# Optimization experiments

Hardware: AMD Instinct MI355X
Metric: run time of the kernel (lower is better)

## Reference

```python
import jax, jax.numpy as jnp
import numpy as np

B, NV, RN, SN = 1, 4, 1024, 128
H = W = 256
C_FEAT = 32   # img_feat_dim
D_VIEW = 32   # view transformer d_model
PE_D = 8      # PE_d_hid
D_RAY = D_VIEW + PE_D  # 40
NHEAD = 8
EPS_LN = 1e-5


def _layernorm(x, g, b):
    m = x.mean(-1, keepdims=True)
    v = ((x - m) ** 2).mean(-1, keepdims=True)
    return (x - m) * jax.lax.rsqrt(v + EPS_LN) * g + b


def _linear_attention(q, k, v):
    # LoFTR kernelized linear attention; q,k,v: (n, L, h, d)
    Q = jax.nn.elu(q) + 1.0
    K = jax.nn.elu(k) + 1.0
    L = v.shape[1]
    KV = jnp.einsum('nshd,nshv->nhdv', K, v / L)
    Z = 1.0 / (jnp.einsum('nlhd,nhd->nlh', Q, K.sum(axis=1)) + 1e-6)
    return jnp.einsum('nlhd,nhdv,nlh->nlhv', Q, KV, Z) * L


def _loftr_self_layer(x, Wq, Wk, Wv, Wm, g1, b1, W1, W2, g2, b2):
    # LoFTREncoderLayer with self-attention (x is both query and source)
    n, L, d = x.shape
    dim = d // NHEAD
    q = (x @ Wq).reshape(n, L, NHEAD, dim)
    k = (x @ Wk).reshape(n, L, NHEAD, dim)
    v = (x @ Wv).reshape(n, L, NHEAD, dim)
    msg = _linear_attention(q, k, v).reshape(n, L, d) @ Wm
    msg = _layernorm(msg, g1, b1)
    msg = jax.nn.relu(jnp.concatenate([x, msg], -1) @ W1) @ W2
    msg = _layernorm(msg, g2, b2)
    return x + msg


def _grid_sample_2d(img, pix):
    # img: (N,C,H,W); pix: (N,RN,SN,2) in pixel coords.
    # bilinear, align_corners=True, zero padding; mask = in-bounds.
    N, C, Hh, Ww = img.shape
    x, y = pix[..., 0], pix[..., 1]
    mask = ((x >= 0) & (x <= Ww - 1) & (y >= 0) & (y <= Hh - 1)).astype(img.dtype)
    x0 = jnp.floor(x)
    y0 = jnp.floor(y)
    flat = img.reshape(N, C, Hh * Ww)

    def gather(ix, iy):
        valid = ((ix >= 0) & (ix < Ww) & (iy >= 0) & (iy < Hh)).astype(img.dtype)
        idx = (jnp.clip(iy, 0, Hh - 1) * Ww + jnp.clip(ix, 0, Ww - 1)).astype(jnp.int32)
        out = jnp.take_along_axis(flat, idx.reshape(N, 1, -1), axis=2)
        return out.reshape(N, C, ix.shape[1], ix.shape[2]) * valid[:, None]

    wx1 = x - x0
    wy1 = y - y0
    out = (gather(x0, y0) * ((1 - wx1) * (1 - wy1))[:, None]
           + gather(x0 + 1, y0) * (wx1 * (1 - wy1))[:, None]
           + gather(x0, y0 + 1) * ((1 - wx1) * wy1)[:, None]
           + gather(x0 + 1, y0 + 1) * (wx1 * wy1)[:, None])
    return out, mask


def _order_posenc(d_hid, n):
    pos = np.arange(n)[:, None].astype(np.float64)
    j = np.arange(d_hid)[None, :]
    tab = pos / np.power(10000.0, 2 * (j // 2) / d_hid)
    tab[:, 0::2] = np.sin(tab[:, 0::2])
    tab[:, 1::2] = np.cos(tab[:, 1::2])
    return jnp.asarray(tab, dtype=jnp.float32)


def _forward(point3D, source_imgs, source_imgs_feat, ref_pose_inv, source_poses_inv,
             source_poses, view_token,
             vt_Wq, vt_Wk, vt_Wv, vt_Wm, vt_g1, vt_b1, vt_W1, vt_W2, vt_g2, vt_b2,
             rt_Wq, rt_Wk, rt_Wv, rt_Wm, rt_g1, rt_b1, rt_W1, rt_W2, rt_g2, rt_b2,
             dm_W1, dm_b1, dm_W2, dm_b2, dm_W3, dm_b3,
             rw_W1, rw_b1, rw_W2, rw_b2, rw_W3, rw_b3):
    b, nv, _, h, w = source_imgs.shape
    _, rn, sn, _ = point3D.shape

    # relative viewing directions (B,NV,RN,SN,3)
    v1 = point3D - ref_pose_inv[:, None, None, :3, -1]
    v2 = point3D[:, None] - source_poses_inv[:, :, None, None, :3, -1]
    v1 = v1 / jnp.linalg.norm(v1, axis=-1, keepdims=True)
    v2 = v2 / jnp.linalg.norm(v2, axis=-1, keepdims=True)
    dir_relative = v1[:, None] - v2

    # project points into all source views: (B,NV,3,RN,SN)
    pts_h = jnp.concatenate([point3D, jnp.ones_like(point3D[..., :1])], -1)
    pip = jnp.einsum('bnij,brsj->bnirs', source_poses, pts_h)[:, :, :3]
    mask_valid_depth = (pip[:, :, 2] > 0).astype(point3D.dtype)
    pix = pip[:, :, :2] / pip[:, :, 2:3]
    grid = jnp.moveaxis(pix, 2, -1).reshape(b * nv, rn, sn, 2)

    feat_s, mask = _grid_sample_2d(source_imgs_feat.reshape(b * nv, -1, h, w), grid)
    rgb_s, _ = _grid_sample_2d(source_imgs.reshape(b * nv, -1, h, w), grid)
    mask = mask.reshape(b, nv, rn, sn) * mask_valid_depth

    # per-point multi-view tokens: (B*RN*SN, NV, C)
    x = feat_s.reshape(b, nv, -1, rn, sn).transpose(0, 3, 4, 1, 2).reshape(b * rn * sn, nv, -1)
    tok = jnp.broadcast_to(view_token, (x.shape[0], 1, view_token.shape[-1]))
    x = jnp.concatenate([tok, x], axis=1)  # prepend view token -> L = NV+1
    x = _loftr_self_layer(x, vt_Wq, vt_Wk, vt_Wv, vt_Wm, vt_g1, vt_b1, vt_W1, vt_W2, vt_g2, vt_b2)

    x1 = jnp.moveaxis(x, 1, 0)          # (NV+1, B*RN*SN, C)
    view_feature = x1[1:]
    x = x1[0].reshape(b * rn, sn, -1)   # token output per sample along ray

    pe = _order_posenc(PE_D, sn)        # (SN, 8)
    x = jnp.concatenate([x, jnp.broadcast_to(pe, (b * rn, sn, PE_D))], -1)
    x = _loftr_self_layer(x, rt_Wq, rt_Wk, rt_Wv, rt_Wm, rt_g1, rt_b1, rt_W1, rt_W2, rt_g2, rt_b2)

    hdm = jax.nn.relu(x @ dm_W1 + dm_b1)
    hdm = jax.nn.relu(hdm @ dm_W2 + dm_b2)
    srdf = hdm @ dm_W3 + dm_b3           # (B*RN, SN, 1)

    # radiance blending weights over views
    vf = view_feature.reshape(nv, b, rn, sn, -1).transpose(1, 2, 3, 0, 4)  # (B,RN,SN,NV,C)
    dr = dir_relative.transpose(0, 2, 3, 1, 4)                             # (B,RN,SN,NV,3)
    xw = jnp.concatenate([vf, dr], -1)
    xw = jax.nn.relu(xw @ rw_W1 + rw_b1)
    xw = jax.nn.relu(xw @ rw_W2 + rw_b2)
    xw = xw @ rw_W3 + rw_b3                                                # (B,RN,SN,NV,1)
    m = mask.transpose(0, 2, 3, 1)[..., None]
    xw = jnp.where(m == 0, -1e9, xw)
    weight = jax.nn.softmax(xw, axis=-2)
    w_bn = weight[..., 0].transpose(0, 3, 1, 2)[:, :, None]                # (B,NV,1,RN,SN)
    radiance = (rgb_s.reshape(b, nv, 3, rn, sn) * w_bn).sum(axis=1)        # (B,3,RN,SN)
    radiance = radiance.transpose(0, 2, 3, 1).reshape(b * rn * sn, 3)
    return radiance, srdf, pip


def setup_inputs() -> dict:
    key = jax.random.key(0)
    ks = jax.random.split(key, 4)
    u = jax.random.uniform(ks[0], (B, RN, SN, 3), dtype=jnp.float32)
    point3D = jnp.concatenate([u[..., :2] - 0.5, u[..., 2:] + 1.0], -1)  # x,y in [-.5,.5], z in [1,2]
    source_imgs = jax.random.normal(ks[1], (B, NV, 3, H, W), dtype=jnp.float32) * 0.5
    source_imgs_feat = jax.random.normal(ks[2], (B, NV, C_FEAT, H, W), dtype=jnp.float32) * 0.5

    f = 200.0
    P = np.array([[f, 0, W / 2, 0], [0, f, H / 2, 0], [0, 0, 1, 0], [0, 0, 0, 1]], np.float32)
    source_poses = jnp.asarray(np.broadcast_to(P, (B, NV, 4, 4)).copy())
    ref_pose_inv = jnp.asarray(np.broadcast_to(np.eye(4, dtype=np.float32), (B, 4, 4)).copy())
    spi = np.broadcast_to(np.eye(4, dtype=np.float32), (B, NV, 4, 4)).copy()
    spi[:, :, 0, 3] = np.linspace(-0.2, 0.2, NV, dtype=np.float32)  # camera centers
    source_poses_inv = jnp.asarray(spi)

    pk = jax.random.split(ks[3], 20)

    def lin(k, i, o):
        return jax.random.normal(k, (i, o), dtype=jnp.float32) * 0.05

    d, dr = D_VIEW, D_RAY
    params = dict(
        view_token=jax.random.normal(pk[0], (1, d), dtype=jnp.float32),
        vt_Wq=lin(pk[1], d, d), vt_Wk=lin(pk[2], d, d), vt_Wv=lin(pk[3], d, d), vt_Wm=lin(pk[4], d, d),
        vt_g1=jnp.ones(d), vt_b1=jnp.zeros(d),
        vt_W1=lin(pk[5], 2 * d, 2 * d), vt_W2=lin(pk[6], 2 * d, d),
        vt_g2=jnp.ones(d), vt_b2=jnp.zeros(d),
        rt_Wq=lin(pk[7], dr, dr), rt_Wk=lin(pk[8], dr, dr), rt_Wv=lin(pk[9], dr, dr), rt_Wm=lin(pk[10], dr, dr),
        rt_g1=jnp.ones(dr), rt_b1=jnp.zeros(dr),
        rt_W1=lin(pk[11], 2 * dr, 2 * dr), rt_W2=lin(pk[12], 2 * dr, dr),
        rt_g2=jnp.ones(dr), rt_b2=jnp.zeros(dr),
        dm_W1=lin(pk[13], dr, 32), dm_b1=jnp.zeros(32),
        dm_W2=lin(pk[14], 32, 16), dm_b2=jnp.zeros(16),
        dm_W3=lin(pk[15], 16, 1), dm_b3=jnp.zeros(1),
        rw_W1=lin(pk[16], d + 3, 16), rw_b1=jnp.zeros(16),
        rw_W2=lin(pk[17], 16, 8), rw_b2=jnp.zeros(8),
        rw_W3=lin(pk[18], 8, 1), rw_b3=jnp.zeros(1),
    )
    out = dict(point3D=point3D, source_imgs=source_imgs, source_imgs_feat=source_imgs_feat,
               ref_pose_inv=ref_pose_inv, source_poses_inv=source_poses_inv,
               source_poses=source_poses)
    out.update(params)
    return out


def reference(point3D, source_imgs, source_imgs_feat, ref_pose_inv, source_poses_inv,
              source_poses, view_token,
              vt_Wq, vt_Wk, vt_Wv, vt_Wm, vt_g1, vt_b1, vt_W1, vt_W2, vt_g2, vt_b2,
              rt_Wq, rt_Wk, rt_Wv, rt_Wm, rt_g1, rt_b1, rt_W1, rt_W2, rt_g2, rt_b2,
              dm_W1, dm_b1, dm_W2, dm_b2, dm_W3, dm_b3,
              rw_W1, rw_b1, rw_W2, rw_b2, rw_W3, rw_b3):
    return _forward(point3D, source_imgs, source_imgs_feat, ref_pose_inv, source_poses_inv,
                    source_poses, view_token,
                    vt_Wq, vt_Wk, vt_Wv, vt_Wm, vt_g1, vt_b1, vt_W1, vt_W2, vt_g2, vt_b2,
                    rt_Wq, rt_Wk, rt_Wv, rt_Wm, rt_g1, rt_b1, rt_W1, rt_W2, rt_g2, rt_b2,
                    dm_W1, dm_b1, dm_W2, dm_b2, dm_W3, dm_b3,
                    rw_W1, rw_b1, rw_W2, rw_b2, rw_W3, rw_b3)
```

## Files before the change

kernel.cpp:

```cpp
#include <hip/hip_runtime.h>
#include <math.h>

#define NPTS   131072
#define NVIEW  4
#define IMH    256
#define IMW    256

#define WS_FEATT   0u
#define WS_IMGT    8388608u
#define WS_X1      9437184u
#define WS_XR      26214400u
#define WS_MSG     31457280u
#define WS_RGB     36700160u
#define WS_DIR     38273024u
#define WS_MASK    39845888u

__device__ __forceinline__ float elup1(float t) { return t > 0.f ? t + 1.f : expf(t); }

__global__ __launch_bounds__(256) void k0_transpose(
    const float* __restrict__ feat, const float* __restrict__ img,
    float* __restrict__ featT, float* __restrict__ imgT)
{
    int tid = blockIdx.x * 256 + threadIdx.x;
    int v = tid >> 16, pix = tid & 65535;
    float buf[32];
#pragma unroll
    for (int c = 0; c < 32; ++c)
        buf[c] = feat[((size_t)(v * 32 + c) << 16) + pix];
    float4* dst = (float4*)(featT + ((size_t)tid << 5));
#pragma unroll
    for (int q = 0; q < 8; ++q)
        dst[q] = make_float4(buf[4*q], buf[4*q+1], buf[4*q+2], buf[4*q+3]);
    float4 rgb;
    rgb.x = img[((size_t)(v * 3 + 0) << 16) + pix];
    rgb.y = img[((size_t)(v * 3 + 1) << 16) + pix];
    rgb.z = img[((size_t)(v * 3 + 2) << 16) + pix];
    rgb.w = 0.f;
    *(float4*)(imgT + ((size_t)tid << 2)) = rgb;
}

__global__ __launch_bounds__(256) void k1_geom_sample(
    const float* __restrict__ p3d, const float* __restrict__ rpi,
    const float* __restrict__ spi, const float* __restrict__ sp,
    const float* __restrict__ featT, const float* __restrict__ imgT,
    float* __restrict__ x1, float* __restrict__ rgbw,
    float* __restrict__ dirw, float* __restrict__ maskw,
    float* __restrict__ outpip)
{
    int tid = blockIdx.x * 256 + threadIdx.x;
    int p = tid >> 2, v = tid & 3;
    float X = p3d[p * 3 + 0], Y = p3d[p * 3 + 1], Z = p3d[p * 3 + 2];

    float a0 = X - rpi[3], a1 = Y - rpi[7], a2 = Z - rpi[11];
    float na = sqrtf(a0 * a0 + a1 * a1 + a2 * a2);
    a0 /= na; a1 /= na; a2 /= na;
    const float* sv = spi + v * 16;
    float b0 = X - sv[3], b1 = Y - sv[7], b2 = Z - sv[11];
    float nb = sqrtf(b0 * b0 + b1 * b1 + b2 * b2);
    b0 /= nb; b1 /= nb; b2 /= nb;
    dirw[(size_t)p * 12 + v * 3 + 0] = a0 - b0;
    dirw[(size_t)p * 12 + v * 3 + 1] = a1 - b1;
    dirw[(size_t)p * 12 + v * 3 + 2] = a2 - b2;

    const float* P = sp + v * 16;
    float pip0 = P[0] * X + P[1] * Y + P[2]  * Z + P[3];
    float pip1 = P[4] * X + P[5] * Y + P[6]  * Z + P[7];
    float pip2 = P[8] * X + P[9] * Y + P[10] * Z + P[11];
    outpip[(size_t)(v * 3 + 0) * NPTS + p] = pip0;
    outpip[(size_t)(v * 3 + 1) * NPTS + p] = pip1;
    outpip[(size_t)(v * 3 + 2) * NPTS + p] = pip2;

    float gx = pip0 / pip2, gy = pip1 / pip2;
    float inb = (gx >= 0.f && gx <= 255.f && gy >= 0.f && gy <= 255.f) ? 1.f : 0.f;
    float mvd = pip2 > 0.f ? 1.f : 0.f;
    maskw[(size_t)p * 4 + v] = inb * mvd;

    float x0f = floorf(gx), y0f = floorf(gy);
    float wx = gx - x0f, wy = gy - y0f;
    int ix0 = (int)x0f, iy0 = (int)y0f;
    float tw[4] = { (1.f-wx)*(1.f-wy), wx*(1.f-wy), (1.f-wx)*wy, wx*wy };
    int tdx[4] = { 0, 1, 0, 1 };
    int tdy[4] = { 0, 0, 1, 1 };

    float facc[32];
#pragma unroll
    for (int c = 0; c < 32; ++c) facc[c] = 0.f;
    float r0 = 0.f, r1 = 0.f, r2 = 0.f;

#pragma unroll
    for (int tno = 0; tno < 4; ++tno) {
        int ix = ix0 + tdx[tno], iy = iy0 + tdy[tno];
        float valid = (ix >= 0 && ix < IMW && iy >= 0 && iy < IMH) ? 1.f : 0.f;
        int cx = min(max(ix, 0), IMW - 1), cy = min(max(iy, 0), IMH - 1);
        float wgt = tw[tno] * valid;
        size_t base = ((size_t)v << 16) + ((size_t)cy << 8) + (size_t)cx;
        const float4* fp = (const float4*)(featT + base * 32);
#pragma unroll
        for (int q = 0; q < 8; ++q) {
            float4 f4 = fp[q];
            facc[4*q+0] += f4.x * wgt; facc[4*q+1] += f4.y * wgt;
            facc[4*q+2] += f4.z * wgt; facc[4*q+3] += f4.w * wgt;
        }
        float4 rp = *(const float4*)(imgT + base * 4);
        r0 += rp.x * wgt; r1 += rp.y * wgt; r2 += rp.z * wgt;
    }

    float4* xd = (float4*)(x1 + ((size_t)p * 4 + v) * 32);
#pragma unroll
    for (int q = 0; q < 8; ++q)
        xd[q] = make_float4(facc[4*q], facc[4*q+1], facc[4*q+2], facc[4*q+3]);
    rgbw[(size_t)p * 12 + v * 3 + 0] = r0;
    rgbw[(size_t)p * 12 + v * 3 + 1] = r1;
    rgbw[(size_t)p * 12 + v * 3 + 2] = r2;
}

#define K2_BLK    128
#define K2_PTS    24
#define K2_GRID   1024
#define K2_NGRP   ((NPTS + K2_PTS - 1) / K2_PTS)

__device__ __forceinline__ void fma4(const float4 xv, const float* __restrict__ w,
                                     const int stride, float* __restrict__ acc)
{
#pragma unroll
    for (int j = 0; j < 32; ++j) acc[j] = fmaf(xv.x, w[j],            acc[j]);
#pragma unroll
    for (int j = 0; j < 32; ++j) acc[j] = fmaf(xv.y, w[stride + j],   acc[j]);
#pragma unroll
    for (int j = 0; j < 32; ++j) acc[j] = fmaf(xv.z, w[2*stride + j], acc[j]);
#pragma unroll
    for (int j = 0; j < 32; ++j) acc[j] = fmaf(xv.w, w[3*stride + j], acc[j]);
}

__global__ __launch_bounds__(K2_BLK) void k2_loftr1(
    float* __restrict__ x1g, const float* __restrict__ vtok,
    const float* __restrict__ Wq, const float* __restrict__ Wk,
    const float* __restrict__ Wv, const float* __restrict__ Wm,
    const float* __restrict__ g1v, const float* __restrict__ b1v,
    const float* __restrict__ W1, const float* __restrict__ W2,
    const float* __restrict__ g2v, const float* __restrict__ b2v,
    float* __restrict__ xr)
{
    __shared__ float shr[8192];

    int t = threadIdx.x;
    int pl = t / 5, l = t - pl * 5;
    bool act = (t < K2_PTS * 5);
    if (!act) { pl = 0; l = 0; }
    const int rowbase = (pl * 5 + l) * 68;

    for (int grp = blockIdx.x; grp < K2_NGRP; grp += gridDim.x) {
        int p = grp * K2_PTS + pl;
        bool valid = act && (p < NPTS);
        int pload = p < NPTS ? p : NPTS - 1;
        const float4* xsrc = (l == 0) ? (const float4*)vtok
                                      : (const float4*)(x1g + ((size_t)pload * 4 + (l - 1)) * 32);

        __syncthreads();

        {
            float acc[32];
#pragma unroll
            for (int j = 0; j < 32; ++j) acc[j] = 0.f;
            for (int g = 0; g < 8; ++g) {
                float4 xv = xsrc[g];
                fma4(xv, &Wk[g * 128], 32, acc);
            }
            if (act) {
                float* krow = &shr[rowbase];
#pragma unroll
                for (int j = 0; j < 32; j += 4)
                    *(float4*)&krow[j] = make_float4(elup1(acc[j]), elup1(acc[j+1]),
                                                     elup1(acc[j+2]), elup1(acc[j+3]));
            }
        }
        {
            float acc[32];
#pragma unroll
            for (int j = 0; j < 32; ++j) acc[j] = 0.f;
            for (int g = 0; g < 8; ++g) {
                float4 xv = xsrc[g];
                fma4(xv, &Wv[g * 128], 32, acc);
            }
            if (act) {
                float* vrow = &shr[rowbase + 32];
#pragma unroll
                for (int j = 0; j < 32; j += 4)
                    *(float4*)&vrow[j] = make_float4(acc[j], acc[j+1], acc[j+2], acc[j+3]);
            }
        }
        __syncthreads();

        float macc[32];
#pragma unroll
        for (int j = 0; j < 32; ++j) macc[j] = 0.f;
        for (int h = 0; h < 8; ++h) {
            float q0 = 0.f, q1 = 0.f, q2 = 0.f, q3 = 0.f;
            for (int g = 0; g < 8; ++g) {
                float4 xv = xsrc[g];
                const float* w = &Wq[g * 128 + h * 4];
                q0 = fmaf(xv.x, w[0],  q0); q1 = fmaf(xv.x, w[1],  q1);
                q2 = fmaf(xv.x, w[2],  q2); q3 = fmaf(xv.x, w[3],  q3);
                q0 = fmaf(xv.y, w[32], q0); q1 = fmaf(xv.y, w[33], q1);
                q2 = fmaf(xv.y, w[34], q2); q3 = fmaf(xv.y, w[35], q3);
                q0 = fmaf(xv.z, w[64], q0); q1 = fmaf(xv.z, w[65], q1);
                q2 = fmaf(xv.z, w[66], q2); q3 = fmaf(xv.z, w[67], q3);
                q0 = fmaf(xv.w, w[96], q0); q1 = fmaf(xv.w, w[97], q1);
                q2 = fmaf(xv.w, w[98], q2); q3 = fmaf(xv.w, w[99], q3);
            }
            q0 = elup1(q0); q1 = elup1(q1); q2 = elup1(q2); q3 = elup1(q3);

            float kvm[16] = {0,0,0,0,0,0,0,0,0,0,0,0,0,0,0,0};
            float ks0 = 0.f, ks1 = 0.f, ks2 = 0.f, ks3 = 0.f;
#pragma unroll
            for (int l2 = 0; l2 < 5; ++l2) {
                const float* row = &shr[(pl * 5 + l2) * 68 + h * 4];
                float4 K4 = *(const float4*)row;
                float4 V4 = *(const float4*)(row + 32);
                kvm[0]  = fmaf(K4.x, V4.x, kvm[0]);  kvm[1]  = fmaf(K4.x, V4.y, kvm[1]);
                kvm[2]  = fmaf(K4.x, V4.z, kvm[2]);  kvm[3]  = fmaf(K4.x, V4.w, kvm[3]);
                kvm[4]  = fmaf(K4.y, V4.x, kvm[4]);  kvm[5]  = fmaf(K4.y, V4.y, kvm[5]);
                kvm[6]  = fmaf(K4.y, V4.z, kvm[6]);  kvm[7]  = fmaf(K4.y, V4.w, kvm[7]);
                kvm[8]  = fmaf(K4.z, V4.x, kvm[8]);  kvm[9]  = fmaf(K4.z, V4.y, kvm[9]);
                kvm[10] = fmaf(K4.z, V4.z, kvm[10]); kvm[11] = fmaf(K4.z, V4.w, kvm[11]);
                kvm[12] = fmaf(K4.w, V4.x, kvm[12]); kvm[13] = fmaf(K4.w, V4.y, kvm[13]);
                kvm[14] = fmaf(K4.w, V4.z, kvm[14]); kvm[15] = fmaf(K4.w, V4.w, kvm[15]);
                ks0 += K4.x; ks1 += K4.y; ks2 += K4.z; ks3 += K4.w;
            }
            float den = 1e-6f + q0*ks0 + q1*ks1 + q2*ks2 + q3*ks3;
            float inv = 1.f / den;
            float o0 = (q0*kvm[0] + q1*kvm[4] + q2*kvm[8]  + q3*kvm[12]) * inv;
            float o1 = (q0*kvm[1] + q1*kvm[5] + q2*kvm[9]  + q3*kvm[13]) * inv;
            float o2 = (q0*kvm[2] + q1*kvm[6] + q2*kvm[10] + q3*kvm[14]) * inv;
            float o3 = (q0*kvm[3] + q1*kvm[7] + q2*kvm[11] + q3*kvm[15]) * inv;

            const float* wm = &Wm[h * 4 * 32];
#pragma unroll
            for (int j = 0; j < 32; ++j) macc[j] = fmaf(o0, wm[j],      macc[j]);
#pragma unroll
            for (int j = 0; j < 32; ++j) macc[j] = fmaf(o1, wm[32 + j], macc[j]);
#pragma unroll
            for (int j = 0; j < 32; ++j) macc[j] = fmaf(o2, wm[64 + j], macc[j]);
#pragma unroll
            for (int j = 0; j < 32; ++j) macc[j] = fmaf(o3, wm[96 + j], macc[j]);
        }

        float msg[32];
        {
            float s1 = 0.f, s2 = 0.f;
#pragma unroll
            for (int j = 0; j < 32; ++j) { s1 += macc[j]; s2 += macc[j] * macc[j]; }
            float m  = s1 * (1.f / 32.f);
            float va = s2 * (1.f / 32.f) - m * m;
            float rs = rsqrtf(va + 1e-5f);
#pragma unroll
            for (int j = 0; j < 32; ++j)
                msg[j] = (macc[j] - m) * rs * g1v[j] + b1v[j];
        }
        __syncthreads();

#pragma unroll
        for (int g = 0; g < 8; ++g)
            *(float4*)&shr[(g * K2_BLK + t) * 4] =
                make_float4(msg[4*g], msg[4*g+1], msg[4*g+2], msg[4*g+3]);

        float oacc[32];
#pragma unroll
        for (int j = 0; j < 32; ++j) oacc[j] = 0.f;
        for (int half = 0; half < 2; ++half) {
            const int j0 = half * 32;
            float hacc[32];
#pragma unroll
            for (int j = 0; j < 32; ++j) hacc[j] = 0.f;
            for (int g = 0; g < 8; ++g) {
                float4 xv = xsrc[g];
                fma4(xv, &W1[(g * 4) * 64 + j0], 64, hacc);
            }
            for (int g = 0; g < 8; ++g) {
                float4 mv = *(const float4*)&shr[(g * K2_BLK + t) * 4];
                fma4(mv, &W1[(32 + g * 4) * 64 + j0], 64, hacc);
            }
#pragma unroll
            for (int j = 0; j < 32; j += 4)
                *(float4*)&shr[4096 + ((j >> 2) * K2_BLK + t) * 4] =
                    make_float4(fmaxf(hacc[j], 0.f),   fmaxf(hacc[j+1], 0.f),
                                fmaxf(hacc[j+2], 0.f), fmaxf(hacc[j+3], 0.f));
            for (int g = 0; g < 8; ++g) {
                float4 hv = *(const float4*)&shr[4096 + (g * K2_BLK + t) * 4];
                fma4(hv, &W2[(j0 + g * 4) * 32], 32, oacc);
            }
        }

        {
            float s1 = 0.f, s2 = 0.f;
#pragma unroll
            for (int j = 0; j < 32; ++j) { s1 += oacc[j]; s2 += oacc[j] * oacc[j]; }
            float m  = s1 * (1.f / 32.f);
            float va = s2 * (1.f / 32.f) - m * m;
            float rs = rsqrtf(va + 1e-5f);

            if (valid) {
                float y[32];
#pragma unroll
                for (int g = 0; g < 8; ++g) {
                    float4 x4 = xsrc[g];
                    y[4*g] = x4.x; y[4*g+1] = x4.y; y[4*g+2] = x4.z; y[4*g+3] = x4.w;
                }
#pragma unroll
                for (int j = 0; j < 32; ++j)
                    y[j] += (oacc[j] - m) * rs * g2v[j] + b2v[j];

                if (l == 0) {
                    float4* dst = (float4*)(xr + (size_t)p * 40);
#pragma unroll
                    for (int g = 0; g < 8; ++g)
                        dst[g] = make_float4(y[4*g], y[4*g+1], y[4*g+2], y[4*g+3]);
                    int sidx = p & 127;
#pragma unroll
                    for (int c = 0; c < 8; ++c) {
                        float den = (c < 2) ? 1.f : (c < 4) ? 10.f : (c < 6) ? 100.f : 1000.f;
                        float arg = (float)sidx / den;
                        xr[(size_t)p * 40 + 32 + c] = (c & 1) ? cosf(arg) : sinf(arg);
                    }
                } else {
                    float4* dst = (float4*)(x1g + ((size_t)p * 4 + (l - 1)) * 32);
#pragma unroll
                    for (int g = 0; g < 8; ++g)
                        dst[g] = make_float4(y[4*g], y[4*g+1], y[4*g+2], y[4*g+3]);
                }
            }
        }
    }
}

__global__ __launch_bounds__(320) void k3a_attn(
    const float* __restrict__ xr,
    const float* __restrict__ Wq, const float* __restrict__ Wk,
    const float* __restrict__ Wv, const float* __restrict__ Wm,
    const float* __restrict__ g1, const float* __restrict__ b1,
    float* __restrict__ msg)
{
    __shared__ float kb[5120];
    __shared__ float vb[5120];
    __shared__ float wb[1600];
    __shared__ float kvb[200];
    __shared__ float ksb[40];
    int t = threadIdx.x, r = blockIdx.x;
    const float* xbase = xr + (size_t)r * 5120;
    int lg = t / 40, c = t % 40;

    for (int i = t; i < 1600; i += 320) wb[i] = Wk[i];
    __syncthreads();
    {
        float acc[16];
#pragma unroll
        for (int i = 0; i < 16; ++i) acc[i] = 0.f;
        for (int kk = 0; kk < 40; ++kk) {
            float w = wb[kk * 40 + c];
#pragma unroll
            for (int i = 0; i < 16; ++i) acc[i] += xbase[(lg * 16 + i) * 40 + kk] * w;
        }
#pragma unroll
        for (int i = 0; i < 16; ++i) kb[(lg * 16 + i) * 40 + c] = elup1(acc[i]);
    }
    __syncthreads();
    for (int i = t; i < 1600; i += 320) wb[i] = Wv[i];
    __syncthreads();
    {
        float acc[16];
#pragma unroll
        for (int i = 0; i < 16; ++i) acc[i] = 0.f;
        for (int kk = 0; kk < 40; ++kk) {
            float w = wb[kk * 40 + c];
#pragma unroll
            for (int i = 0; i < 16; ++i) acc[i] += xbase[(lg * 16 + i) * 40 + kk] * w;
        }
#pragma unroll
        for (int i = 0; i < 16; ++i) vb[(lg * 16 + i) * 40 + c] = acc[i];
    }
    __syncthreads();
    if (t < 200) {
        int h = t / 25, e = (t / 5) % 5, d = t % 5;
        float kv = 0.f, ks = 0.f;
        for (int s2 = 0; s2 < 128; ++s2) {
            float kvv = kb[s2 * 40 + h * 5 + e];
            float vv  = vb[s2 * 40 + h * 5 + d];
            kv += kvv * vv; ks += kvv;
        }
        kvb[t] = kv;
        if (d == 0) ksb[h * 5 + e] = ks;
    }
    __syncthreads();
    for (int i = t; i < 1600; i += 320) wb[i] = Wq[i];
    __syncthreads();
    {
        float acc[16];
#pragma unroll
        for (int i = 0; i < 16; ++i) acc[i] = 0.f;
        for (int kk = 0; kk < 40; ++kk) {
            float w = wb[kk * 40 + c];
#pragma unroll
            for (int i = 0; i < 16; ++i) acc[i] += xbase[(lg * 16 + i) * 40 + kk] * w;
        }
#pragma unroll
        for (int i = 0; i < 16; ++i) kb[(lg * 16 + i) * 40 + c] = elup1(acc[i]);
    }
    __syncthreads();
    {
        int h = c / 5, d = c % 5;
#pragma unroll 4
        for (int i = 0; i < 16; ++i) {
            int l = lg * 16 + i;
            float den = 1e-6f, o = 0.f;
#pragma unroll
            for (int e = 0; e < 5; ++e) {
                float q = kb[l * 40 + h * 5 + e];
                den += q * ksb[h * 5 + e];
                o   += q * kvb[h * 25 + e * 5 + d];
            }
            vb[l * 40 + c] = o / den;
        }
    }
    __syncthreads();
    for (int i = t; i < 1600; i += 320) wb[i] = Wm[i];
    __syncthreads();
    {
        float acc[16];
#pragma unroll
        for (int i = 0; i < 16; ++i) acc[i] = 0.f;
        for (int kk = 0; kk < 40; ++kk) {
            float w = wb[kk * 40 + c];
#pragma unroll
            for (int i = 0; i < 16; ++i) acc[i] += vb[(lg * 16 + i) * 40 + kk] * w;
        }
#pragma unroll
        for (int i = 0; i < 16; ++i) kb[(lg * 16 + i) * 40 + c] = acc[i];
    }
    __syncthreads();
    if (t < 128) {
        float s1 = 0.f, s2v = 0.f;
        for (int j = 0; j < 40; ++j) { float x = kb[t * 40 + j]; s1 += x; s2v += x * x; }
        float m = s1 * (1.f / 40.f), va = s2v * (1.f / 40.f) - m * m;
        float rs = rsqrtf(va + 1e-5f);
        for (int j = 0; j < 40; ++j)
            msg[((size_t)r * 128 + t) * 40 + j] = (kb[t * 40 + j] - m) * rs * g1[j] + b1[j];
    }
}

__global__ __launch_bounds__(320) void k3b_ffn(
    float* __restrict__ xr, const float* __restrict__ msg,
    const float* __restrict__ W1, const float* __restrict__ W2,
    const float* __restrict__ g2, const float* __restrict__ b2)
{
    __shared__ float hb[10240];
    __shared__ float wb[3200];
    int t = threadIdx.x, r = blockIdx.x;
    int lg = t / 40, c = t % 40;
    const float* xbase = xr + (size_t)r * 5120;
    const float* mbase = msg + (size_t)r * 5120;

    float hA[16], hB[16];
#pragma unroll
    for (int i = 0; i < 16; ++i) { hA[i] = 0.f; hB[i] = 0.f; }

    for (int i = t; i < 3200; i += 320) wb[i] = W1[i];
    __syncthreads();
    for (int kk = 0; kk < 40; ++kk) {
        float wa = wb[kk * 80 + c], wbb = wb[kk * 80 + c + 40];
#pragma unroll
        for (int i = 0; i < 16; ++i) {
            float xv = xbase[(lg * 16 + i) * 40 + kk];
            hA[i] += xv * wa; hB[i] += xv * wbb;
        }
    }
    __syncthreads();
    for (int i = t; i < 3200; i += 320) wb[i] = W1[3200 + i];
    __syncthreads();
    for (int kk = 0; kk < 40; ++kk) {
        float wa = wb[kk * 80 + c], wbb = wb[kk * 80 + c + 40];
#pragma unroll
        for (int i = 0; i < 16; ++i) {
            float mv = mbase[(lg * 16 + i) * 40 + kk];
            hA[i] += mv * wa; hB[i] += mv * wbb;
        }
    }
#pragma unroll
    for (int i = 0; i < 16; ++i) {
        hb[(lg * 16 + i) * 80 + c]      = fmaxf(hA[i], 0.f);
        hb[(lg * 16 + i) * 80 + c + 40] = fmaxf(hB[i], 0.f);
    }
    __syncthreads();
    for (int i = t; i < 3200; i += 320) wb[i] = W2[i];
    __syncthreads();
    float oa[16];
#pragma unroll
    for (int i = 0; i < 16; ++i) oa[i] = 0.f;
    for (int kk = 0; kk < 80; ++kk) {
        float w = wb[kk * 40 + c];
#pragma unroll
        for (int i = 0; i < 16; ++i) oa[i] += hb[(lg * 16 + i) * 80 + kk] * w;
    }
    __syncthreads();
#pragma unroll
    for (int i = 0; i < 16; ++i) hb[(lg * 16 + i) * 40 + c] = oa[i];
    __syncthreads();
    if (t < 128) {
        float s1 = 0.f, s2v = 0.f;
        for (int j = 0; j < 40; ++j) { float x = hb[t * 40 + j]; s1 += x; s2v += x * x; }
        float m = s1 * (1.f / 40.f), va = s2v * (1.f / 40.f) - m * m;
        float rs = rsqrtf(va + 1e-5f);
        for (int j = 0; j < 40; ++j) {
            float y = xbase[t * 40 + j] + (hb[t * 40 + j] - m) * rs * g2[j] + b2[j];
            xr[(size_t)r * 5120 + t * 40 + j] = y;
        }
    }
}

__global__ __launch_bounds__(256) void k4_dm(
    const float* __restrict__ xr,
    const float* __restrict__ W1, const float* __restrict__ b1,
    const float* __restrict__ W2, const float* __restrict__ b2,
    const float* __restrict__ W3, const float* __restrict__ b3,
    float* __restrict__ out1)
{
    __shared__ float s[1857];
    int t = threadIdx.x;
    for (int i = t; i < 1280; i += 256) s[i] = W1[i];
    if (t < 32) s[1280 + t] = b1[t];
    for (int i = t; i < 512; i += 256) s[1312 + i] = W2[i];
    if (t < 16) { s[1824 + t] = b2[t]; s[1840 + t] = W3[t]; }
    if (t == 0) s[1856] = b3[0];
    __syncthreads();

    int p = blockIdx.x * 256 + t;
    float x[40];
    const float4* xp = (const float4*)(xr + (size_t)p * 40);
#pragma unroll
    for (int i = 0; i < 10; ++i) {
        float4 v4 = xp[i];
        x[4*i] = v4.x; x[4*i+1] = v4.y; x[4*i+2] = v4.z; x[4*i+3] = v4.w;
    }
    float h1[32];
#pragma unroll
    for (int j = 0; j < 32; ++j) h1[j] = s[1280 + j];
    for (int k = 0; k < 40; ++k) {
        float xv = x[k];
#pragma unroll
        for (int j = 0; j < 32; ++j) h1[j] += xv * s[k * 32 + j];
    }
#pragma unroll
    for (int j = 0; j < 32; ++j) h1[j] = fmaxf(h1[j], 0.f);
    float h2[16];
#pragma unroll
    for (int j = 0; j < 16; ++j) h2[j] = s[1824 + j];
    for (int k = 0; k < 32; ++k) {
        float hv = h1[k];
#pragma unroll
        for (int j = 0; j < 16; ++j) h2[j] += hv * s[1312 + k * 16 + j];
    }
    float o = s[1856];
#pragma unroll
    for (int j = 0; j < 16; ++j) o += fmaxf(h2[j], 0.f) * s[1840 + j];
    out1[p] = o;
}

__global__ __launch_bounds__(256) void k5_rw(
    const float* __restrict__ vf, const float* __restrict__ dirw,
    const float* __restrict__ maskw, const float* __restrict__ rgbw,
    const float* __restrict__ W1, const float* __restrict__ b1,
    const float* __restrict__ W2, const float* __restrict__ b2,
    const float* __restrict__ W3, const float* __restrict__ b3,
    float* __restrict__ out0)
{
    __shared__ float s[721];
    int t = threadIdx.x;
    for (int i = t; i < 560; i += 256) s[i] = W1[i];
    if (t < 16) s[560 + t] = b1[t];
    if (t < 128) s[576 + t] = W2[t];
    if (t < 8) { s[704 + t] = b2[t]; s[712 + t] = W3[t]; }
    if (t == 0) s[720] = b3[0];
    __syncthreads();

    int p = blockIdx.x * 256 + t;
    float xw[4];
#pragma unroll
    for (int v = 0; v < 4; ++v) {
        float in[35];
        const float4* vp = (const float4*)(vf + ((size_t)p * 4 + v) * 32);
#pragma unroll
        for (int q = 0; q < 8; ++q) {
            float4 f4 = vp[q];
            in[4*q] = f4.x; in[4*q+1] = f4.y; in[4*q+2] = f4.z; in[4*q+3] = f4.w;
        }
        in[32] = dirw[(size_t)p * 12 + v * 3 + 0];
        in[33] = dirw[(size_t)p * 12 + v * 3 + 1];
        in[34] = dirw[(size_t)p * 12 + v * 3 + 2];
        float h1[16];
#pragma unroll
        for (int j = 0; j < 16; ++j) h1[j] = s[560 + j];
        for (int k = 0; k < 35; ++k) {
            float xv = in[k];
#pragma unroll
            for (int j = 0; j < 16; ++j) h1[j] += xv * s[k * 16 + j];
        }
        float h2[8];
#pragma unroll
        for (int j = 0; j < 8; ++j) h2[j] = s[704 + j];
        for (int k = 0; k < 16; ++k) {
            float hv = fmaxf(h1[k], 0.f);
#pragma unroll
            for (int j = 0; j < 8; ++j) h2[j] += hv * s[576 + k * 8 + j];
        }
        float o = s[720];
#pragma unroll
        for (int j = 0; j < 8; ++j) o += fmaxf(h2[j], 0.f) * s[712 + j];
        xw[v] = (maskw[(size_t)p * 4 + v] == 0.f) ? -1e9f : o;
    }
    float m = fmaxf(fmaxf(xw[0], xw[1]), fmaxf(xw[2], xw[3]));
    float e0 = expf(xw[0] - m), e1 = expf(xw[1] - m), e2 = expf(xw[2] - m), e3 = expf(xw[3] - m);
    float inv = 1.f / (e0 + e1 + e2 + e3);
    float w4[4] = { e0 * inv, e1 * inv, e2 * inv, e3 * inv };
    float r0 = 0.f, r1 = 0.f, r2 = 0.f;
#pragma unroll
    for (int v = 0; v < 4; ++v) {
        r0 += rgbw[(size_t)p * 12 + v * 3 + 0] * w4[v];
        r1 += rgbw[(size_t)p * 12 + v * 3 + 1] * w4[v];
        r2 += rgbw[(size_t)p * 12 + v * 3 + 2] * w4[v];
    }
    out0[(size_t)p * 3 + 0] = r0;
    out0[(size_t)p * 3 + 1] = r1;
    out0[(size_t)p * 3 + 2] = r2;
}

extern "C" void kernel_launch(void* const* d_in, const int* in_sizes, int n_in,
                              void* d_out, int out_size, void* d_ws, size_t ws_size,
                              hipStream_t stream) {
    (void)in_sizes; (void)n_in; (void)out_size; (void)ws_size;
    const float* p3d   = (const float*)d_in[0];
    const float* imgs  = (const float*)d_in[1];
    const float* feat  = (const float*)d_in[2];
    const float* rpi   = (const float*)d_in[3];
    const float* spi   = (const float*)d_in[4];
    const float* sp    = (const float*)d_in[5];
    const float* vtok  = (const float*)d_in[6];
    const float* vtWq  = (const float*)d_in[7];
    const float* vtWk  = (const float*)d_in[8];
    const float* vtWv  = (const float*)d_in[9];
    const float* vtWm  = (const float*)d_in[10];
    const float* vtg1  = (const float*)d_in[11];
    const float* vtb1  = (const float*)d_in[12];
    const float* vtW1  = (const float*)d_in[13];
    const float* vtW2  = (const float*)d_in[14];
    const float* vtg2  = (const float*)d_in[15];
    const float* vtb2  = (const float*)d_in[16];
    const float* rtWq  = (const float*)d_in[17];
    const float* rtWk  = (const float*)d_in[18];
    const float* rtWv  = (const float*)d_in[19];
    const float* rtWm  = (const float*)d_in[20];
    const float* rtg1  = (const float*)d_in[21];
    const float* rtb1  = (const float*)d_in[22];
    const float* rtW1  = (const float*)d_in[23];
    const float* rtW2  = (const float*)d_in[24];
    const float* rtg2  = (const float*)d_in[25];
    const float* rtb2  = (const float*)d_in[26];
    const float* dmW1  = (const float*)d_in[27];
    const float* dmb1  = (const float*)d_in[28];
    const float* dmW2  = (const float*)d_in[29];
    const float* dmb2  = (const float*)d_in[30];
    const float* dmW3  = (const float*)d_in[31];
    const float* dmb3  = (const float*)d_in[32];
    const float* rwW1  = (const float*)d_in[33];
    const float* rwb1  = (const float*)d_in[34];
    const float* rwW2  = (const float*)d_in[35];
    const float* rwb2  = (const float*)d_in[36];
    const float* rwW3  = (const float*)d_in[37];
    const float* rwb3  = (const float*)d_in[38];

    float* out  = (float*)d_out;
    float* out0 = out;
    float* out1 = out + 393216;
    float* out2 = out + 524288;

    float* ws    = (float*)d_ws;
    float* featT = ws + WS_FEATT;
    float* imgT  = ws + WS_IMGT;
    float* x1    = ws + WS_X1;
    float* xr    = ws + WS_XR;
    float* msg   = ws + WS_MSG;
    float* rgbw  = ws + WS_RGB;
    float* dirw  = ws + WS_DIR;
    float* maskw = ws + WS_MASK;

    k0_transpose<<<dim3(1024), dim3(256), 0, stream>>>(feat, imgs, featT, imgT);
    k1_geom_sample<<<dim3(2048), dim3(256), 0, stream>>>(p3d, rpi, spi, sp, featT, imgT,
                                                         x1, rgbw, dirw, maskw, out2);
    k2_loftr1<<<dim3(K2_GRID), dim3(K2_BLK), 0, stream>>>(x1, vtok, vtWq, vtWk, vtWv, vtWm,
                                                    vtg1, vtb1, vtW1, vtW2, vtg2, vtb2, xr);
    k3a_attn<<<dim3(1024), dim3(320), 0, stream>>>(xr, rtWq, rtWk, rtWv, rtWm, rtg1, rtb1, msg);
    k3b_ffn<<<dim3(1024), dim3(320), 0, stream>>>(xr, msg, rtW1, rtW2, rtg2, rtb2);
    k4_dm<<<dim3(512), dim3(256), 0, stream>>>(xr, dmW1, dmb1, dmW2, dmb2, dmW3, dmb3, out1);
    k5_rw<<<dim3(512), dim3(256), 0, stream>>>(x1, dirw, maskw, rgbw,
                                               rwW1, rwb1, rwW2, rwb2, rwW3, rwb3, out0);
}
```

Measured before the change: 1.130 ms.

## Restructure ray-transformer attention and FFN kernels to one thread per sample

Rewrites k3a_attn and k3b_ffn so each thread owns one sample and holds its 40-wide rows in registers, doing the projections with wave-uniform weight loads from global/scalar memory instead of staging weights in LDS. K and V are written transposed into padded LDS so the per-head KV reduction can use float4 reads. Block size drops from 320 to 128 threads, and most syncthreads and LDS traffic are removed. In exchange, register pressure rises sharply (arrays of 40 floats, with two or three live at once) and weights are re-read per thread, which may cut occupancy.

```diff
diff --git a/kernel.cpp b/kernel.cpp
--- a/kernel.cpp
+++ b/kernel.cpp
@@ -130,6 +130,19 @@
     for (int j = 0; j < 32; ++j) acc[j] = fmaf(xv.z, w[2*stride + j], acc[j]);
 #pragma unroll
     for (int j = 0; j < 32; ++j) acc[j] = fmaf(xv.w, w[3*stride + j], acc[j]);
+}
+
+__device__ __forceinline__ void fma40(const float4 xv, const float* __restrict__ w,
+                                      const int stride, float* __restrict__ acc)
+{
+#pragma unroll
+    for (int j = 0; j < 40; ++j) acc[j] = fmaf(xv.x, w[j],            acc[j]);
+#pragma unroll
+    for (int j = 0; j < 40; ++j) acc[j] = fmaf(xv.y, w[stride + j],   acc[j]);
+#pragma unroll
+    for (int j = 0; j < 40; ++j) acc[j] = fmaf(xv.z, w[2*stride + j], acc[j]);
+#pragma unroll
+    for (int j = 0; j < 40; ++j) acc[j] = fmaf(xv.w, w[3*stride + j], acc[j]);
 }
 
 __global__ __launch_bounds__(K2_BLK) void k2_loftr1(
@@ -333,186 +346,177 @@
     }
 }
 
-__global__ __launch_bounds__(320) void k3a_attn(
+#define KT_STRIDE 132
+__global__ __launch_bounds__(128) void k3a_attn(
     const float* __restrict__ xr,
     const float* __restrict__ Wq, const float* __restrict__ Wk,
     const float* __restrict__ Wv, const float* __restrict__ Wm,
     const float* __restrict__ g1, const float* __restrict__ b1,
     float* __restrict__ msg)
 {
-    __shared__ float kb[5120];
-    __shared__ float vb[5120];
-    __shared__ float wb[1600];
+    __shared__ float KT[40 * KT_STRIDE];
+    __shared__ float VT[40 * KT_STRIDE];
     __shared__ float kvb[200];
     __shared__ float ksb[40];
+
     int t = threadIdx.x, r = blockIdx.x;
-    const float* xbase = xr + (size_t)r * 5120;
-    int lg = t / 40, c = t % 40;
-
-    for (int i = t; i < 1600; i += 320) wb[i] = Wk[i];
+    const float4* x4 = (const float4*)(xr + ((size_t)r * 128 + t) * 40);
+
+    {
+        float acc[40];
+#pragma unroll
+        for (int j = 0; j < 40; ++j) acc[j] = 0.f;
+        for (int g = 0; g < 10; ++g)
+            fma40(x4[g], &Wk[g * 160], 40, acc);
+#pragma unroll
+        for (int j = 0; j < 40; ++j) KT[j * KT_STRIDE + t] = elup1(acc[j]);
+    }
+    {
+        float acc[40];
+#pragma unroll
+        for (int j = 0; j < 40; ++j) acc[j] = 0.f;
+        for (int g = 0; g < 10; ++g)
+            fma40(x4[g], &Wv[g * 160], 40, acc);
+#pragma unroll
+        for (int j = 0; j < 40; ++j) VT[j * KT_STRIDE + t] = acc[j];
+    }
     __syncthreads();
+
     {
-        float acc[16];
-#pragma unroll
-        for (int i = 0; i < 16; ++i) acc[i] = 0.f;
-        for (int kk = 0; kk < 40; ++kk) {
-            float w = wb[kk * 40 + c];
-#pragma unroll
-            for (int i = 0; i < 16; ++i) acc[i] += xbase[(lg * 16 + i) * 40 + kk] * w;
-        }
-#pragma unroll
-        for (int i = 0; i < 16; ++i) kb[(lg * 16 + i) * 40 + c] = elup1(acc[i]);
+        int lane = t & 63, wid = t >> 6;
+        if (lane < 20) {
+            int idx = wid * 20 + lane;
+            int h = idx / 5;
+            float ks = 0.f;
+            float kv0 = 0.f, kv1 = 0.f, kv2 = 0.f, kv3 = 0.f, kv4 = 0.f;
+            const float* kr = &KT[idx * KT_STRIDE];
+            const float* v0 = &VT[(h * 5 + 0) * KT_STRIDE];
+            const float* v1 = &VT[(h * 5 + 1) * KT_STRIDE];
+            const float* v2 = &VT[(h * 5 + 2) * KT_STRIDE];
+            const float* v3 = &VT[(h * 5 + 3) * KT_STRIDE];
+            const float* v4 = &VT[(h * 5 + 4) * KT_STRIDE];
+            for (int s = 0; s < 128; s += 4) {
+                float4 K4 = *(const float4*)&kr[s];
+                float4 A = *(const float4*)&v0[s];
+                float4 B = *(const float4*)&v1[s];
+                float4 C = *(const float4*)&v2[s];
+                float4 D = *(const float4*)&v3[s];
+                float4 E = *(const float4*)&v4[s];
+                ks  += K4.x + K4.y + K4.z + K4.w;
+                kv0 += K4.x*A.x + K4.y*A.y + K4.z*A.z + K4.w*A.w;
+                kv1 += K4.x*B.x + K4.y*B.y + K4.z*B.z + K4.w*B.w;
+                kv2 += K4.x*C.x + K4.y*C.y + K4.z*C.z + K4.w*C.w;
+                kv3 += K4.x*D.x + K4.y*D.y + K4.z*D.z + K4.w*D.w;
+                kv4 += K4.x*E.x + K4.y*E.y + K4.z*E.z + K4.w*E.w;
+            }
+            ksb[idx] = ks;
+            kvb[idx * 5 + 0] = kv0; kvb[idx * 5 + 1] = kv1;
+            kvb[idx * 5 + 2] = kv2; kvb[idx * 5 + 3] = kv3;
+            kvb[idx * 5 + 4] = kv4;
+        }
     }
     __syncthreads();
-    for (int i = t; i < 1600; i += 320) wb[i] = Wv[i];
-    __syncthreads();
+
+    float o[40];
     {
-        float acc[16];
-#pragma unroll
-        for (int i = 0; i < 16; ++i) acc[i] = 0.f;
-        for (int kk = 0; kk < 40; ++kk) {
-            float w = wb[kk * 40 + c];
-#pragma unroll
-            for (int i = 0; i < 16; ++i) acc[i] += xbase[(lg * 16 + i) * 40 + kk] * w;
-        }
-#pragma unroll
-        for (int i = 0; i < 16; ++i) vb[(lg * 16 + i) * 40 + c] = acc[i];
-    }
-    __syncthreads();
-    if (t < 200) {
-        int h = t / 25, e = (t / 5) % 5, d = t % 5;
-        float kv = 0.f, ks = 0.f;
-        for (int s2 = 0; s2 < 128; ++s2) {
-            float kvv = kb[s2 * 40 + h * 5 + e];
-            float vv  = vb[s2 * 40 + h * 5 + d];
-            kv += kvv * vv; ks += kvv;
-        }
-        kvb[t] = kv;
-        if (d == 0) ksb[h * 5 + e] = ks;
-    }
-    __syncthreads();
-    for (int i = t; i < 1600; i += 320) wb[i] = Wq[i];
-    __syncthreads();
+        float q[40];
+#pragma unroll
+        for (int j = 0; j < 40; ++j) q[j] = 0.f;
+        for (int g = 0; g < 10; ++g)
+            fma40(x4[g], &Wq[g * 160], 40, q);
+#pragma unroll
+        for (int j = 0; j < 40; ++j) q[j] = elup1(q[j]);
+
+#pragma unroll
+        for (int h = 0; h < 8; ++h) {
+            float den = 1e-6f;
+#pragma unroll
+            for (int e = 0; e < 5; ++e) den += q[h*5+e] * ksb[h*5+e];
+            float inv = 1.f / den;
+#pragma unroll
+            for (int d = 0; d < 5; ++d) {
+                float val = 0.f;
+#pragma unroll
+                for (int e = 0; e < 5; ++e)
+                    val += q[h*5+e] * kvb[(h*5+e)*5 + d];
+                o[h*5+d] = val * inv;
+            }
+        }
+    }
+    float macc[40];
+#pragma unroll
+    for (int j = 0; j < 40; ++j) macc[j] = 0.f;
+#pragma unroll
+    for (int g = 0; g < 10; ++g) {
+        float4 ov = make_float4(o[4*g], o[4*g+1], o[4*g+2], o[4*g+3]);
+        fma40(ov, &Wm[g * 160], 40, macc);
+    }
     {
-        float acc[16];
-#pragma unroll
-        for (int i = 0; i < 16; ++i) acc[i] = 0.f;
-        for (int kk = 0; kk < 40; ++kk) {
-            float w = wb[kk * 40 + c];
-#pragma unroll
-            for (int i = 0; i < 16; ++i) acc[i] += xbase[(lg * 16 + i) * 40 + kk] * w;
-        }
-#pragma unroll
-        for (int i = 0; i < 16; ++i) kb[(lg * 16 + i) * 40 + c] = elup1(acc[i]);
-    }
-    __syncthreads();
-    {
-        int h = c / 5, d = c % 5;
-#pragma unroll 4
-        for (int i = 0; i < 16; ++i) {
-            int l = lg * 16 + i;
-            float den = 1e-6f, o = 0.f;
-#pragma unroll
-            for (int e = 0; e < 5; ++e) {
-                float q = kb[l * 40 + h * 5 + e];
-                den += q * ksb[h * 5 + e];
-                o   += q * kvb[h * 25 + e * 5 + d];
-            }
-            vb[l * 40 + c] = o / den;
-        }
-    }
-    __syncthreads();
-    for (int i = t; i < 1600; i += 320) wb[i] = Wm[i];
-    __syncthreads();
-    {
-        float acc[16];
-#pragma unroll
-        for (int i = 0; i < 16; ++i) acc[i] = 0.f;
-        for (int kk = 0; kk < 40; ++kk) {
-            float w = wb[kk * 40 + c];
-#pragma unroll
-            for (int i = 0; i < 16; ++i) acc[i] += vb[(lg * 16 + i) * 40 + kk] * w;
-        }
-#pragma unroll
-        for (int i = 0; i < 16; ++i) kb[(lg * 16 + i) * 40 + c] = acc[i];
-    }
-    __syncthreads();
-    if (t < 128) {
-        float s1 = 0.f, s2v = 0.f;
-        for (int j = 0; j < 40; ++j) { float x = kb[t * 40 + j]; s1 += x; s2v += x * x; }
-        float m = s1 * (1.f / 40.f), va = s2v * (1.f / 40.f) - m * m;
+        float s1 = 0.f, s2 = 0.f;
+#pragma unroll
+        for (int j = 0; j < 40; ++j) { s1 += macc[j]; s2 += macc[j] * macc[j]; }
+        float mu = s1 * (1.f / 40.f);
+        float va = s2 * (1.f / 40.f) - mu * mu;
         float rs = rsqrtf(va + 1e-5f);
+#pragma unroll
         for (int j = 0; j < 40; ++j)
-            msg[((size_t)r * 128 + t) * 40 + j] = (kb[t * 40 + j] - m) * rs * g1[j] + b1[j];
-    }
-}
-
-__global__ __launch_bounds__(320) void k3b_ffn(
+            macc[j] = (macc[j] - mu) * rs * g1[j] + b1[j];
+    }
+    float4* md = (float4*)(msg + ((size_t)r * 128 + t) * 40);
+#pragma unroll
+    for (int g = 0; g < 10; ++g)
+        md[g] = make_float4(macc[4*g], macc[4*g+1], macc[4*g+2], macc[4*g+3]);
+}
+
+__global__ __launch_bounds__(128) void k3b_ffn(
     float* __restrict__ xr, const float* __restrict__ msg,
     const float* __restrict__ W1, const float* __restrict__ W2,
     const float* __restrict__ g2, const float* __restrict__ b2)
 {
-    __shared__ float hb[10240];
-    __shared__ float wb[3200];
-    int t = threadIdx.x, r = blockIdx.x;
-    int lg = t / 40, c = t % 40;
-    const float* xbase = xr + (size_t)r * 5120;
-    const float* mbase = msg + (size_t)r * 5120;
-
-    float hA[16], hB[16];
-#pragma unroll
-    for (int i = 0; i < 16; ++i) { hA[i] = 0.f; hB[i] = 0.f; }
-
-    for (int i = t; i < 3200; i += 320) wb[i] = W1[i];
-    __syncthreads();
-    for (int kk = 0; kk < 40; ++kk) {
-        float wa = wb[kk * 80 + c], wbb = wb[kk * 80 + c + 40];
-#pragma unroll
-        for (int i = 0; i < 16; ++i) {
-            float xv = xbase[(lg * 16 + i) * 40 + kk];
-            hA[i] += xv * wa; hB[i] += xv * wbb;
-        }
-    }
-    __syncthreads();
-    for (int i = t; i < 3200; i += 320) wb[i] = W1[3200 + i];
-    __syncthreads();
-    for (int kk = 0; kk < 40; ++kk) {
-        float wa = wb[kk * 80 + c], wbb = wb[kk * 80 + c + 40];
-#pragma unroll
-        for (int i = 0; i < 16; ++i) {
-            float mv = mbase[(lg * 16 + i) * 40 + kk];
-            hA[i] += mv * wa; hB[i] += mv * wbb;
-        }
-    }
-#pragma unroll
-    for (int i = 0; i < 16; ++i) {
-        hb[(lg * 16 + i) * 80 + c]      = fmaxf(hA[i], 0.f);
-        hb[(lg * 16 + i) * 80 + c + 40] = fmaxf(hB[i], 0.f);
-    }
-    __syncthreads();
-    for (int i = t; i < 3200; i += 320) wb[i] = W2[i];
-    __syncthreads();
-    float oa[16];
-#pragma unroll
-    for (int i = 0; i < 16; ++i) oa[i] = 0.f;
-    for (int kk = 0; kk < 80; ++kk) {
-        float w = wb[kk * 40 + c];
-#pragma unroll
-        for (int i = 0; i < 16; ++i) oa[i] += hb[(lg * 16 + i) * 80 + kk] * w;
-    }
-    __syncthreads();
-#pragma unroll
-    for (int i = 0; i < 16; ++i) hb[(lg * 16 + i) * 40 + c] = oa[i];
-    __syncthreads();
-    if (t < 128) {
-        float s1 = 0.f, s2v = 0.f;
-        for (int j = 0; j < 40; ++j) { float x = hb[t * 40 + j]; s1 += x; s2v += x * x; }
-        float m = s1 * (1.f / 40.f), va = s2v * (1.f / 40.f) - m * m;
-        float rs = rsqrtf(va + 1e-5f);
-        for (int j = 0; j < 40; ++j) {
-            float y = xbase[t * 40 + j] + (hb[t * 40 + j] - m) * rs * g2[j] + b2[j];
-            xr[(size_t)r * 5120 + t * 40 + j] = y;
-        }
+    int p = blockIdx.x * 128 + threadIdx.x;
+    const float4* x4 = (const float4*)(xr + (size_t)p * 40);
+    const float4* m4 = (const float4*)(msg + (size_t)p * 40);
+
+    float oacc[40];
+#pragma unroll
+    for (int j = 0; j < 40; ++j) oacc[j] = 0.f;
+
+#pragma unroll
+    for (int half = 0; half < 2; ++half) {
+        const int j0 = half * 40;
+        float hacc[40];
+#pragma unroll
+        for (int j = 0; j < 40; ++j) hacc[j] = 0.f;
+        for (int g = 0; g < 10; ++g)
+            fma40(x4[g], &W1[(g * 4) * 80 + j0], 80, hacc);
+        for (int g = 0; g < 10; ++g)
+            fma40(m4[g], &W1[(40 + g * 4) * 80 + j0], 80, hacc);
+#pragma unroll
+        for (int j = 0; j < 40; ++j) hacc[j] = fmaxf(hacc[j], 0.f);
+#pragma unroll
+        for (int g = 0; g < 10; ++g) {
+            float4 hv = make_float4(hacc[4*g], hacc[4*g+1], hacc[4*g+2], hacc[4*g+3]);
+            fma40(hv, &W2[(j0 + g * 4) * 40], 40, oacc);
+        }
+    }
+
+    float s1 = 0.f, s2 = 0.f;
+#pragma unroll
+    for (int j = 0; j < 40; ++j) { s1 += oacc[j]; s2 += oacc[j] * oacc[j]; }
+    float mu = s1 * (1.f / 40.f);
+    float va = s2 * (1.f / 40.f) - mu * mu;
+    float rs = rsqrtf(va + 1e-5f);
+
+    float4* dst = (float4*)(xr + (size_t)p * 40);
+#pragma unroll
+    for (int g = 0; g < 10; ++g) {
+        float4 xv = x4[g];
+        float4 o4;
+        o4.x = xv.x + (oacc[4*g+0] - mu) * rs * g2[4*g+0] + b2[4*g+0];
+        o4.y = xv.y + (oacc[4*g+1] - mu) * rs * g2[4*g+1] + b2[4*g+1];
+        o4.z = xv.z + (oacc[4*g+2] - mu) * rs * g2[4*g+2] + b2[4*g+2];
+        o4.w = xv.w + (oacc[4*g+3] - mu) * rs * g2[4*g+3] + b2[4*g+3];
+        dst[g] = o4;
     }
 }
 
@@ -696,8 +700,8 @@
                                                          x1, rgbw, dirw, maskw, out2);
     k2_loftr1<<<dim3(K2_GRID), dim3(K2_BLK), 0, stream>>>(x1, vtok, vtWq, vtWk, vtWv, vtWm,
                                                     vtg1, vtb1, vtW1, vtW2, vtg2, vtb2, xr);
-    k3a_attn<<<dim3(1024), dim3(320), 0, stream>>>(xr, rtWq, rtWk, rtWv, rtWm, rtg1, rtb1, msg);
-    k3b_ffn<<<dim3(1024), dim3(320), 0, stream>>>(xr, msg, rtW1, rtW2, rtg2, rtb2);
+    k3a_attn<<<dim3(1024), dim3(128), 0, stream>>>(xr, rtWq, rtWk, rtWv, rtWm, rtg1, rtb1, msg);
+    k3b_ffn<<<dim3(1024), dim3(128), 0, stream>>>(xr, msg, rtW1, rtW2, rtg2, rtb2);
     k4_dm<<<dim3(512), dim3(256), 0, stream>>>(xr, dmW1, dmb1, dmW2, dmb2, dmW3, dmb3, out1);
     k5_rw<<<dim3(512), dim3(256), 0, stream>>>(x1, dirw, maskw, rgbw,
                                                rwW1, rwb1, rwW2, rwb2, rwW3, rwb3, out0);
```

Result: faster. 1.010 ms (-10.6%).
